# Kernel tuning notes

Measured on AMD Instinct MI355X. Metric: run time of the kernel, lower is better.

Reference implementation:

```python
import jax, jax.numpy as jnp
import numpy as np
import math

B, N, R = 1024, 50, 1000
N_POIS = 50000
D = 128
K_T = 64
K_D = 64
T_MAX = 10080.0
D_MAX = 200.0
EARTH_RADIUS_KM = 6371.0
DEG2RAD = math.pi / 180.0


def _interp_scalar(table, x):
    # Linear interpolation into 1-D table [K]; x are bin positions in [0, K-1].
    K = table.shape[0]
    x = jnp.clip(x, 0.0, K - 1 - 1e-06)
    k = jnp.floor(x).astype(jnp.int32)
    frac = x - k.astype(x.dtype)
    return (1.0 - frac) * table[k] + frac * table[jnp.minimum(k + 1, K - 1)]


def _haversine_km(lat1, lon1, lat2, lon2):
    dlat = (lat2 - lat1) * DEG2RAD
    dlon = (lon2 - lon1) * DEG2RAD
    a = jnp.sin(dlat / 2) ** 2 + jnp.cos(lat1 * DEG2RAD) * jnp.cos(lat2 * DEG2RAD) * jnp.sin(dlon / 2) ** 2
    a = jnp.clip(a, 0.0, 1.0)
    return EARTH_RADIUS_KM * 2.0 * jnp.arcsin(jnp.sqrt(a))


def setup_inputs() -> dict:
    key = jax.random.key(0)
    ks = jax.random.split(key, 16)
    poi_idx = jax.random.randint(ks[0], (B, N), 0, N_POIS)
    hour_of_week = jax.random.randint(ks[1], (B, N), 0, 169)
    lat = jax.random.uniform(ks[2], (B, N), jnp.float32)  # ~1 degree spread => up to ~150 km pairwise
    lon = jax.random.uniform(ks[3], (B, N), jnp.float32)
    t_min = jax.random.uniform(ks[4], (B, N), jnp.float32) * T_MAX
    region_centroids = jax.random.uniform(ks[5], (R, 2), jnp.float32)
    poi_emb = 0.02 * jax.random.normal(ks[6], (N_POIS + 1, D), jnp.float32)
    poi_emb = poi_emb.at[N_POIS].set(0.0)  # padding row
    time_emb = 0.02 * jax.random.normal(ks[7], (169, D), jnp.float32)
    time_emb = time_emb.at[0].set(0.0)  # padding row
    E_t = 0.1 * jax.random.normal(ks[8], (K_T,), jnp.float32)
    E_d = 0.1 * jax.random.normal(ks[9], (K_D,), jnp.float32)
    E_d_match = 0.1 * jax.random.normal(ks[10], (K_D,), jnp.float32)
    region_emb = 0.02 * jax.random.normal(ks[11], (R, D), jnp.float32)
    Wq = jax.random.normal(ks[12], (D, D), jnp.float32) / math.sqrt(D)
    Wk = jax.random.normal(ks[13], (D, D), jnp.float32) / math.sqrt(D)
    Wv = jax.random.normal(ks[14], (D, D), jnp.float32) / math.sqrt(D)
    return dict(poi_idx=poi_idx, hour_of_week=hour_of_week, lat=lat, lon=lon, t_min=t_min,
                region_centroids=region_centroids, poi_emb=poi_emb, time_emb=time_emb,
                E_t=E_t, E_d=E_d, E_d_match=E_d_match, region_emb=region_emb,
                Wq=Wq, Wk=Wk, Wv=Wv)


def reference(poi_idx, hour_of_week, lat, lon, t_min, region_centroids,
              poi_emb, time_emb, E_t, E_d, E_d_match, region_emb, Wq, Wk, Wv):
    pad_mask = poi_idx < 0  # [B, n]
    poi_safe = jnp.where(pad_mask, N_POIS, poi_idx)
    hour_safe = jnp.where(pad_mask, 0, hour_of_week)
    x = poi_emb[poi_safe] + time_emb[hour_safe]  # [B, n, D]

    # pairwise trajectory intervals [B, n, n]
    dt = jnp.abs(t_min[:, :, None] - t_min[:, None, :])
    dd = _haversine_km(lat[:, :, None], lon[:, :, None], lat[:, None, :], lon[:, None, :])
    valid = (~pad_mask).astype(x.dtype)
    valid_pair = valid[:, :, None] * valid[:, None, :]
    dt = dt * valid_pair
    dd = dd * valid_pair

    # _PairwiseBias: scalar table interpolation bias
    t_bin = jnp.clip(dt, 0.0, T_MAX) / T_MAX * (K_T - 1)
    d_bin = jnp.clip(dd, 0.0, D_MAX) / D_MAX * (K_D - 1)
    bias = _interp_scalar(E_t, t_bin) + _interp_scalar(E_d, d_bin)  # [B, n, n]

    # _SelfAttn (single head, no LN/residual, dropout=0)
    Q = x @ Wq.T
    K_ = x @ Wk.T
    V = x @ Wv.T
    scores = jnp.einsum('bnd,bmd->bnm', Q, K_) / math.sqrt(D) + bias
    scores = jnp.where(pad_mask[:, None, :], -jnp.inf, scores)
    attn = jnp.nan_to_num(jax.nn.softmax(scores, axis=-1), nan=0.0)
    S = attn @ V  # [B, n, D]

    # _MatchingLayer
    cand_lat = region_centroids[:, 0]
    cand_lon = region_centroids[:, 1]
    dd_m = _haversine_km(lat[:, :, None], lon[:, :, None], cand_lat[None, None, :], cand_lon[None, None, :])  # [B, n, R]
    dbin_m = jnp.clip(dd_m, 0.0, D_MAX) / D_MAX * (K_D - 1)
    bias_match = _interp_scalar(E_d_match, dbin_m)
    m_scores = jnp.einsum('bnd,rd->bnr', S, region_emb) / math.sqrt(D) + bias_match
    m_scores = jnp.where(pad_mask[:, :, None], -jnp.inf, m_scores)
    m_attn = jnp.nan_to_num(jax.nn.softmax(m_scores, axis=1), nan=0.0)  # softmax over trajectory dim
    scores_safe = jnp.where(pad_mask[:, :, None], 0.0, m_scores)
    return jnp.sum(m_attn * scores_safe, axis=1)  # [B, R]
```

## Files before the change

kernel.cpp:

```cpp
#include <hip/hip_runtime.h>
#include <hip/hip_bf16.h>
#include <math.h>

constexpr int BB    = 1024;
constexpr int NN    = 50;
constexpr int RR    = 1000;
constexpr int DD    = 128;
constexpr int NPOIS = 50000;
#define DEG2RADF  0.017453292519943295f
#define KHALF     0.008726646259971648f
#define RSQRTD    0.08838834764831845f
#define LOG2E     1.4426950408889634f
#define LN2       0.6931471805599453f
#define DBIN_C0   4013.7373f
#define DBIN_C1   668.95621f
#define TBIN_SC   0.00625f
#define PENAL     -1.0e30f

typedef __attribute__((ext_vector_type(8))) short bfrag8;
typedef __attribute__((ext_vector_type(4))) float f32x4;

__device__ __forceinline__ int swz128(int row, int k) {
    return row * 128 + ((((k) >> 3) ^ (row & 7)) << 3) + (k & 7);
}

__device__ __forceinline__ unsigned short f2bf(float x) {
    union { __hip_bfloat16 h; unsigned short u; } cv;
    cv.h = __float2bfloat16(x);
    return cv.u;
}

__device__ __forceinline__ float exp2_asm(float x) {
    float r;
    asm("v_exp_f32 %0, %1" : "=v"(r) : "v"(x));
    return r;
}

__device__ __forceinline__ float fract_asm(float x) {
    float r;
    asm("v_fract_f32 %0, %1" : "=v"(r) : "v"(x));
    return r;
}

__device__ __forceinline__ float cos_small(float x) {
    float x2 = x * x;
    return 1.0f - 0.5f * x2 + 0.041666667f * x2 * x2;
}

__global__ void prep_mg(const float* __restrict__ Wq, const float* __restrict__ Wk,
                        const float* __restrict__ Wv, const float* __restrict__ Re,
                        unsigned short* __restrict__ Mt, unsigned short* __restrict__ Gp) {
    int k = threadIdx.x;
    if (blockIdx.x < DD) {
        int c = blockIdx.x;
        float s0 = 0.f, s1 = 0.f, s2 = 0.f, s3 = 0.f;
        for (int d = 0; d < DD; d += 4) {
            s0 += Wq[(d + 0) * DD + k] * Wk[(d + 0) * DD + c];
            s1 += Wq[(d + 1) * DD + k] * Wk[(d + 1) * DD + c];
            s2 += Wq[(d + 2) * DD + k] * Wk[(d + 2) * DD + c];
            s3 += Wq[(d + 3) * DD + k] * Wk[(d + 3) * DD + c];
        }
        Mt[c * DD + k] = f2bf((s0 + s1 + s2 + s3) * (RSQRTD * LOG2E));
    } else {
        int r = blockIdx.x - DD;
        float val = 0.f;
        if (r < RR) {
            float s0 = 0.f, s1 = 0.f, s2 = 0.f, s3 = 0.f;
            for (int d = 0; d < DD; d += 4) {
                s0 += Wv[(d + 0) * DD + k] * Re[r * DD + d + 0];
                s1 += Wv[(d + 1) * DD + k] * Re[r * DD + d + 1];
                s2 += Wv[(d + 2) * DD + k] * Re[r * DD + d + 2];
                s3 += Wv[(d + 3) * DD + k] * Re[r * DD + d + 3];
            }
            val = (s0 + s1 + s2 + s3) * (RSQRTD * LOG2E);
        }
        int rt = r >> 6, widr = (r >> 4) & 3, colr = r & 15;
        int ks = k >> 5, quad = (k >> 3) & 3, k7 = k & 7;
        int lane = quad * 16 + colr;
        Gp[((((rt * 16 + widr * 4 + ks) * 64) + lane) << 3) + k7] = f2bf(val);
    }
}

__global__ __launch_bounds__(256) void stan_attn(
    const int* __restrict__ poi_idx, const int* __restrict__ hourw,
    const float* __restrict__ lat, const float* __restrict__ lon,
    const float* __restrict__ tmin,
    const float* __restrict__ poi_emb, const float* __restrict__ time_emb,
    const float* __restrict__ Et_g, const float* __restrict__ Ed_g,
    const unsigned short* __restrict__ Mtb, unsigned short* __restrict__ Zw) {
    __shared__ short xs[64 * 128];
    __shared__ union {
        short ys[64 * 128];
        short ps[64 * 64];
    } u2;
    __shared__ float2 Et2[64], Ed2[64];
    __shared__ float4 bnfo[64];
    __shared__ float  jpen[64];

    const int b = blockIdx.x, tid = threadIdx.x;
    const int wid = tid >> 6, lane = tid & 63;
    const int quad = lane >> 4, colr = lane & 15;

    if (tid < 64) {
        int kk = tid > 62 ? 62 : tid;
        float t0 = Et_g[kk] * LOG2E, t1 = Et_g[kk + 1] * LOG2E;
        float d0 = Ed_g[kk] * LOG2E, d1 = Ed_g[kk + 1] * LOG2E;
        Et2[tid] = make_float2(t0, t1 - t0);
        Ed2[tid] = make_float2(d0, d1 - d0);
        if (tid < NN) {
            int p = poi_idx[b * NN + tid];
            float la = lat[b * NN + tid], lo = lon[b * NN + tid];
            bnfo[tid] = make_float4(la * KHALF, lo * KHALF,
                                    cos_small(la * DEG2RADF),
                                    tmin[b * NN + tid] * TBIN_SC);
            jpen[tid] = (p < 0) ? PENAL : 0.f;
        } else {
            bnfo[tid] = make_float4(0.f, 0.f, 1.f, 0.f);
            jpen[tid] = PENAL;
        }
    }
    __syncthreads();

    for (int idx = tid; idx < 64 * 64; idx += 256) {
        int n = idx >> 6, c2 = idx & 63;
        float2 v = make_float2(0.f, 0.f);
        if (n < NN) {
            int p = poi_idx[b * NN + n];
            int pd = (p < 0);
            int ps_ = pd ? NPOIS : p;
            int hs  = pd ? 0 : hourw[b * NN + n];
            float2 pe = ((const float2*)(poi_emb  + (size_t)ps_ * DD))[c2];
            float2 te = ((const float2*)(time_emb + (size_t)hs  * DD))[c2];
            v = make_float2(pe.x + te.x, pe.y + te.y);
        }
        unsigned pack = (unsigned)f2bf(v.x) | ((unsigned)f2bf(v.y) << 16);
        ((unsigned*)xs)[n * 64 + (((c2 >> 2) ^ (n & 7)) << 2) + (c2 & 3)] = pack;
    }
    __syncthreads();

    const int q8    = (quad ^ (colr & 3)) * 8;
    const int kx    = (colr & 4) * 8;
    const int xbase = colr * 128 + q8;
    const int xe = xbase + kx, xo = xbase - kx;

    {
        f32x4 accY[2][4];
        #pragma unroll
        for (int ct = 0; ct < 2; ct++)
            #pragma unroll
            for (int mt = 0; mt < 4; mt++) accY[ct][mt] = (f32x4){0.f, 0.f, 0.f, 0.f};
        #pragma unroll
        for (int ks = 0; ks < 4; ks++) {
            const int k0 = ks * 32 + quad * 8;
            const int xoff = ((ks & 1) ? xo : xe) + ks * 32;
            bfrag8 av[4], bv[2];
            #pragma unroll
            for (int mt = 0; mt < 4; mt++)
                av[mt] = *(const bfrag8*)(&xs[xoff + mt * 2048]);
            #pragma unroll
            for (int ct = 0; ct < 2; ct++) {
                int c = wid * 32 + ct * 16 + colr;
                bv[ct] = *(const bfrag8*)(Mtb + (size_t)c * DD + k0);
            }
            #pragma unroll
            for (int ct = 0; ct < 2; ct++)
                #pragma unroll
                for (int mt = 0; mt < 4; mt++)
                    accY[ct][mt] = __builtin_amdgcn_mfma_f32_16x16x32_bf16(
                        av[mt], bv[ct], accY[ct][mt], 0, 0, 0);
        }
        #pragma unroll
        for (int ct = 0; ct < 2; ct++)
            #pragma unroll
            for (int mt = 0; mt < 4; mt++)
                #pragma unroll
                for (int reg = 0; reg < 4; reg++) {
                    int m = mt * 16 + quad * 4 + reg;
                    int c = wid * 32 + ct * 16 + colr;
                    u2.ys[swz128(m, c)] = (short)f2bf(accY[ct][mt][reg]);
                }
    }
    __syncthreads();

    const int i = wid * 16 + colr;
    const int ybase = xbase + wid * 2048;
    const int ye = ybase + kx, yo = ybase - kx;
    f32x4 accS[4];
    #pragma unroll
    for (int mt = 0; mt < 4; mt++) accS[mt] = (f32x4){0.f, 0.f, 0.f, 0.f};
    #pragma unroll
    for (int ks = 0; ks < 4; ks++) {
        const int yoff = ((ks & 1) ? yo : ye) + ks * 32;
        const int xoff = ((ks & 1) ? xo : xe) + ks * 32;
        bfrag8 bv = *(const bfrag8*)(&u2.ys[yoff]);
        #pragma unroll
        for (int mt = 0; mt < 4; mt++) {
            bfrag8 av = *(const bfrag8*)(&xs[xoff + mt * 2048]);
            accS[mt] = __builtin_amdgcn_mfma_f32_16x16x32_bf16(
                av, bv, accS[mt], 0, 0, 0);
        }
    }
    __syncthreads();

    {
        const float4 bi = bnfo[i];
        float sv[14];
        #pragma unroll
        for (int mt = 0; mt < 4; mt++) {
            const int nregs = (mt == 3) ? 2 : 4;
            #pragma unroll
            for (int reg = 0; reg < nregs; reg++) {
                int j = mt * 16 + quad * 4 + reg;
                float4 bj = bnfo[j];
                float tb = fabsf(bi.w - bj.w);
                int   kt = (int)tb;
                float ft = fract_asm(tb);
                float2 et = Et2[kt];
                float bt = fmaf(ft, et.y, et.x);
                float du = bi.x - bj.x, dv = bi.y - bj.y;
                float a = fmaf((bi.z * bj.z) * dv, dv, du * du);
                float x = __builtin_amdgcn_sqrtf(a);
                float db = x * fmaf(a, DBIN_C1, DBIN_C0);
                int   kd = (int)db;
                float fd = fract_asm(db);
                float2 ed = Ed2[kd];
                float bd = fmaf(fd, ed.y, ed.x);
                sv[mt * 4 + reg] = (accS[mt][reg] + bt) + (bd + jpen[j]);
            }
        }
        float mx = sv[0];
        #pragma unroll
        for (int t = 1; t < 14; t++) mx = fmaxf(mx, sv[t]);
        mx = fmaxf(mx, __shfl_xor(mx, 16, 64));
        mx = fmaxf(mx, __shfl_xor(mx, 32, 64));
        float l = 0.f;
        #pragma unroll
        for (int t = 0; t < 14; t++) {
            float p = exp2_asm(sv[t] - mx);
            sv[t] = p;
            l += p;
        }
        l += __shfl_xor(l, 16, 64);
        l += __shfl_xor(l, 32, 64);
        float rl = __builtin_amdgcn_rcpf(l);
        #pragma unroll
        for (int mt = 0; mt < 4; mt++)
            #pragma unroll
            for (int rp = 0; rp < 2; rp++) {
                int j0 = mt * 16 + quad * 4 + rp * 2;
                unsigned pack;
                if (mt == 3 && rp == 1) {
                    pack = 0u;
                } else {
                    unsigned lo = f2bf(sv[mt * 4 + rp * 2]     * rl);
                    unsigned hi = f2bf(sv[mt * 4 + rp * 2 + 1] * rl);
                    pack = lo | (hi << 16);
                }
                ((unsigned*)u2.ps)[i * 32 + (((j0 >> 3) ^ (i & 7)) << 2) + ((j0 & 7) >> 1)]
                    = pack;
            }
    }
    __syncthreads();

    {
        f32x4 accZ[2][4];
        #pragma unroll
        for (int nt = 0; nt < 2; nt++)
            #pragma unroll
            for (int mt = 0; mt < 4; mt++) accZ[nt][mt] = (f32x4){0.f, 0.f, 0.f, 0.f};
        union BF { unsigned u[4]; bfrag8 v; };
        const int pbase = colr * 64 + q8;
        const int pe = pbase + kx, po = pbase - kx;
        #pragma unroll
        for (int ks = 0; ks < 2; ks++) {
            const int k0 = ks * 32 + quad * 8;
            const int poff = ((ks & 1) ? po : pe) + ks * 32;
            bfrag8 av[4];
            #pragma unroll
            for (int mt = 0; mt < 4; mt++)
                av[mt] = *(const bfrag8*)(&u2.ps[poff + mt * 1024]);
            BF bvx[2];
            #pragma unroll
            for (int nt = 0; nt < 2; nt++) {
                int d = wid * 32 + nt * 16 + colr;
                #pragma unroll
                for (int t2 = 0; t2 < 4; t2++) {
                    unsigned lo = (unsigned short)xs[swz128(k0 + 2 * t2,     d)];
                    unsigned hi = (unsigned short)xs[swz128(k0 + 2 * t2 + 1, d)];
                    bvx[nt].u[t2] = lo | (hi << 16);
                }
            }
            #pragma unroll
            for (int nt = 0; nt < 2; nt++)
                #pragma unroll
                for (int mt = 0; mt < 4; mt++)
                    accZ[nt][mt] = __builtin_amdgcn_mfma_f32_16x16x32_bf16(
                        av[mt], bvx[nt].v, accZ[nt][mt], 0, 0, 0);
        }
        unsigned short* Zb = Zw + (size_t)b * NN * DD;
        #pragma unroll
        for (int mt = 0; mt < 4; mt++)
            #pragma unroll
            for (int reg = 0; reg < 4; reg++) {
                int ii = mt * 16 + quad * 4 + reg;
                if (ii < NN) {
                    #pragma unroll
                    for (int nt = 0; nt < 2; nt++) {
                        int d = wid * 32 + nt * 16 + colr;
                        Zb[(size_t)ii * DD + d] = f2bf(accZ[nt][mt][reg]);
                    }
                }
            }
    }
}

__global__ __launch_bounds__(256, 8) void stan_match(
    const unsigned short* __restrict__ Zw, const unsigned short* __restrict__ Gp,
    const float* __restrict__ cent, const float* __restrict__ Em_g,
    const int* __restrict__ poi_idx,
    const float* __restrict__ lat, const float* __restrict__ lon,
    float* __restrict__ out) {
    __shared__ short  As[64 * 128];
    __shared__ float2 Em2[64];
    __shared__ float4 Rnfo[64];
    __shared__ float4 bnfo[64];

    const int tid = threadIdx.x;
    const int b = blockIdx.x, rt = blockIdx.y;
    const int rbase = rt * 64;
    const int wid  = tid >> 6, lane = tid & 63;
    const int quad = lane >> 4, colr = lane & 15;

    if (tid < 64) {
        int kk = tid > 62 ? 62 : tid;
        float e0 = Em_g[kk] * LOG2E, e1 = Em_g[kk + 1] * LOG2E;
        Em2[tid] = make_float2(e0, e1 - e0);
        int rc = rbase + tid; if (rc > RR - 1) rc = RR - 1;
        float la = cent[rc * 2], lo = cent[rc * 2 + 1];
        Rnfo[tid] = make_float4(la * KHALF, lo * KHALF, cos_small(la * DEG2RADF), 0.f);
        if (tid < NN) {
            float bla = lat[b * NN + tid], blo = lon[b * NN + tid];
            float pen = (poi_idx[b * NN + tid] < 0) ? PENAL : 0.f;
            bnfo[tid] = make_float4(bla * KHALF, blo * KHALF,
                                    cos_small(bla * DEG2RADF), pen);
        } else {
            bnfo[tid] = make_float4(0.f, 0.f, 1.f, PENAL);
        }
    }
    {
        const int row = tid >> 2;
        uint4 z4 = make_uint4(0, 0, 0, 0);
        uint4 a0 = z4, a1 = z4, a2 = z4, a3 = z4;
        if (row < NN) {
            const uint4* src = (const uint4*)(Zw + (size_t)b * NN * DD + row * DD
                                              + (tid & 3) * 32);
            a0 = src[0]; a1 = src[1]; a2 = src[2]; a3 = src[3];
        }
        const int jb = (tid & 3) * 4, rx = row & 7;
        uint4* dstA = (uint4*)As;
        dstA[row * 16 + ((jb + 0) ^ rx)] = a0;
        dstA[row * 16 + ((jb + 1) ^ rx)] = a1;
        dstA[row * 16 + ((jb + 2) ^ rx)] = a2;
        dstA[row * 16 + ((jb + 3) ^ rx)] = a3;
    }

    const unsigned short* Gf = Gp + ((size_t)((rt * 16 + wid * 4) * 64 + lane) << 3);
    bfrag8 bfv[4];
    #pragma unroll
    for (int ks = 0; ks < 4; ks++)
        bfv[ks] = *(const bfrag8*)(Gf + ks * 512);

    __syncthreads();

    const int rL = wid * 16 + colr;
    const int r  = rbase + rL;

    const int q8    = (quad ^ (colr & 3)) * 8;
    const int kx    = (colr & 4) * 8;
    const int abase = colr * 128 + q8;
    const int ae = abase + kx, ao = abase - kx;

    f32x4 acc[4];
    #pragma unroll
    for (int mt = 0; mt < 4; mt++) acc[mt] = (f32x4){0.f, 0.f, 0.f, 0.f};

    #pragma unroll
    for (int ks = 0; ks < 4; ks++) {
        const int aoff = ((ks & 1) ? ao : ae) + ks * 32;
        #pragma unroll
        for (int mt = 0; mt < 4; mt++) {
            bfrag8 af = *(const bfrag8*)(&As[aoff + mt * 2048]);
            acc[mt] = __builtin_amdgcn_mfma_f32_16x16x32_bf16(af, bfv[ks], acc[mt], 0, 0, 0);
        }
    }

    const float4 rv = Rnfo[rL];
    float s[14];
    #pragma unroll
    for (int mt = 0; mt < 4; mt++) {
        const int nregs = (mt == 3) ? 2 : 4;
        #pragma unroll
        for (int reg = 0; reg < nregs; reg++) {
            int n = mt * 16 + quad * 4 + reg;
            float4 bn = bnfo[n];
            float du = bn.x - rv.x, dv = bn.y - rv.y;
            float a = fmaf((bn.z * rv.z) * dv, dv, du * du);
            float x = __builtin_amdgcn_sqrtf(a);
            float db = x * fmaf(a, DBIN_C1, DBIN_C0);
            int   kd = (int)db;
            float fd = fract_asm(db);
            float2 ed = Em2[kd];
            float bias = fmaf(fd, ed.y, ed.x);
            s[mt * 4 + reg] = (acc[mt][reg] + bias) + bn.w;
        }
    }
    float m = s[0];
    #pragma unroll
    for (int t = 1; t < 14; t++) m = fmaxf(m, s[t]);
    m = fmaxf(m, __shfl_xor(m, 16, 64));
    m = fmaxf(m, __shfl_xor(m, 32, 64));
    float l = 0.f, aw = 0.f;
    #pragma unroll
    for (int t = 0; t < 14; t++) {
        float p = exp2_asm(s[t] - m);
        l += p;
        aw = fmaf(p, s[t], aw);
    }
    l  += __shfl_xor(l, 16, 64); aw += __shfl_xor(aw, 16, 64);
    l  += __shfl_xor(l, 32, 64); aw += __shfl_xor(aw, 32, 64);
    if (quad == 0 && r < RR)
        out[(size_t)b * RR + r] = aw * __builtin_amdgcn_rcpf(l) * LN2;
}

extern "C" void kernel_launch(void* const* d_in, const int* in_sizes, int n_in,
                              void* d_out, int out_size, void* d_ws, size_t ws_size,
                              hipStream_t stream) {
    const int*   poi_idx  = (const int*)d_in[0];
    const int*   hourw    = (const int*)d_in[1];
    const float* lat      = (const float*)d_in[2];
    const float* lon      = (const float*)d_in[3];
    const float* tmin     = (const float*)d_in[4];
    const float* cent     = (const float*)d_in[5];
    const float* poi_emb  = (const float*)d_in[6];
    const float* time_emb = (const float*)d_in[7];
    const float* E_t      = (const float*)d_in[8];
    const float* E_d      = (const float*)d_in[9];
    const float* E_dm     = (const float*)d_in[10];
    const float* Remb     = (const float*)d_in[11];
    const float* Wq       = (const float*)d_in[12];
    const float* Wk       = (const float*)d_in[13];
    const float* Wv       = (const float*)d_in[14];
    float* out            = (float*)d_out;

    unsigned short* Mtb = (unsigned short*)d_ws;
    unsigned short* Gpb = Mtb + DD * DD;
    unsigned short* Zw  = Gpb + (size_t)1024 * DD;

    prep_mg<<<dim3(DD + 1024), DD, 0, stream>>>(Wq, Wk, Wv, Remb, Mtb, Gpb);
    stan_attn<<<dim3(BB), 256, 0, stream>>>(poi_idx, hourw, lat, lon, tmin,
                                            poi_emb, time_emb, E_t, E_d, Mtb, Zw);
    stan_match<<<dim3(BB, 16), 256, 0, stream>>>(Zw, Gpb, cent, E_dm, poi_idx, lat, lon, out);
}
```

Measured before the change: 184.8 us.

## Store Z in MFMA fragment order so match kernel reads A directly from global

The attention kernel now writes its per-batch Z output zero-padded to 64 rows and pre-swizzled into the exact bf16 MFMA A-fragment layout. The match kernel drops its LDS staging buffer and copy, and loads each A fragment straight from global memory with one 16-byte load per lane. This removes 16KB of LDS per block and the LDS write/read round trip, which should allow higher occupancy. In exchange, each of the 16 region-tile blocks per batch now rereads Z from global or L2, and the workspace per batch grows from 50 to 64 rows.

Measured after the change: 213.7 us. +15.7%, slower.

```diff
diff --git a/kernel.cpp b/kernel.cpp
--- a/kernel.cpp
+++ b/kernel.cpp
@@ -87,7 +87,7 @@
     const float* __restrict__ tmin,
     const float* __restrict__ poi_emb, const float* __restrict__ time_emb,
     const float* __restrict__ Et_g, const float* __restrict__ Ed_g,
-    const unsigned short* __restrict__ Mtb, unsigned short* __restrict__ Zw) {
+    const unsigned short* __restrict__ Mtb, unsigned short* __restrict__ Zp) {
     __shared__ short xs[64 * 128];
     __shared__ union {
         short ys[64 * 128];
@@ -297,30 +297,29 @@
                     accZ[nt][mt] = __builtin_amdgcn_mfma_f32_16x16x32_bf16(
                         av[mt], bvx[nt].v, accZ[nt][mt], 0, 0, 0);
         }
-        unsigned short* Zb = Zw + (size_t)b * NN * DD;
+        unsigned short* Zb = Zp + ((size_t)b << 13);
         #pragma unroll
         for (int mt = 0; mt < 4; mt++)
             #pragma unroll
             for (int reg = 0; reg < 4; reg++) {
                 int ii = mt * 16 + quad * 4 + reg;
-                if (ii < NN) {
-                    #pragma unroll
-                    for (int nt = 0; nt < 2; nt++) {
-                        int d = wid * 32 + nt * 16 + colr;
-                        Zb[(size_t)ii * DD + d] = f2bf(accZ[nt][mt][reg]);
-                    }
+                #pragma unroll
+                for (int nt = 0; nt < 2; nt++) {
+                    float zv = (ii < NN) ? accZ[nt][mt][reg] : 0.f;
+                    int qc = nt * 2 + (colr >> 3);
+                    Zb[(mt * 4 + wid) * 512 + (qc * 16 + quad * 4 + reg) * 8 + (colr & 7)]
+                        = f2bf(zv);
                 }
             }
     }
 }
 
 __global__ __launch_bounds__(256, 8) void stan_match(
-    const unsigned short* __restrict__ Zw, const unsigned short* __restrict__ Gp,
+    const unsigned short* __restrict__ Zp, const unsigned short* __restrict__ Gp,
     const float* __restrict__ cent, const float* __restrict__ Em_g,
     const int* __restrict__ poi_idx,
     const float* __restrict__ lat, const float* __restrict__ lon,
     float* __restrict__ out) {
-    __shared__ short  As[64 * 128];
     __shared__ float2 Em2[64];
     __shared__ float4 Rnfo[64];
     __shared__ float4 bnfo[64];
@@ -330,6 +329,12 @@
     const int rbase = rt * 64;
     const int wid  = tid >> 6, lane = tid & 63;
     const int quad = lane >> 4, colr = lane & 15;
+
+    const unsigned short* Gf = Gp + ((size_t)((rt * 16 + wid * 4) * 64 + lane) << 3);
+    bfrag8 bfv[4];
+    #pragma unroll
+    for (int ks = 0; ks < 4; ks++)
+        bfv[ks] = *(const bfrag8*)(Gf + ks * 512);
 
     if (tid < 64) {
         int kk = tid > 62 ? 62 : tid;
@@ -347,38 +352,12 @@
             bnfo[tid] = make_float4(0.f, 0.f, 1.f, PENAL);
         }
     }
-    {
-        const int row = tid >> 2;
-        uint4 z4 = make_uint4(0, 0, 0, 0);
-        uint4 a0 = z4, a1 = z4, a2 = z4, a3 = z4;
-        if (row < NN) {
-            const uint4* src = (const uint4*)(Zw + (size_t)b * NN * DD + row * DD
-                                              + (tid & 3) * 32);
-            a0 = src[0]; a1 = src[1]; a2 = src[2]; a3 = src[3];
-        }
-        const int jb = (tid & 3) * 4, rx = row & 7;
-        uint4* dstA = (uint4*)As;
-        dstA[row * 16 + ((jb + 0) ^ rx)] = a0;
-        dstA[row * 16 + ((jb + 1) ^ rx)] = a1;
-        dstA[row * 16 + ((jb + 2) ^ rx)] = a2;
-        dstA[row * 16 + ((jb + 3) ^ rx)] = a3;
-    }
-
-    const unsigned short* Gf = Gp + ((size_t)((rt * 16 + wid * 4) * 64 + lane) << 3);
-    bfrag8 bfv[4];
-    #pragma unroll
-    for (int ks = 0; ks < 4; ks++)
-        bfv[ks] = *(const bfrag8*)(Gf + ks * 512);
-
     __syncthreads();
 
     const int rL = wid * 16 + colr;
     const int r  = rbase + rL;
 
-    const int q8    = (quad ^ (colr & 3)) * 8;
-    const int kx    = (colr & 4) * 8;
-    const int abase = colr * 128 + q8;
-    const int ae = abase + kx, ao = abase - kx;
+    const unsigned short* Ab = Zp + ((size_t)b << 13) + lane * 8;
 
     f32x4 acc[4];
     #pragma unroll
@@ -386,10 +365,9 @@
 
     #pragma unroll
     for (int ks = 0; ks < 4; ks++) {
-        const int aoff = ((ks & 1) ? ao : ae) + ks * 32;
         #pragma unroll
         for (int mt = 0; mt < 4; mt++) {
-            bfrag8 af = *(const bfrag8*)(&As[aoff + mt * 2048]);
+            bfrag8 af = *(const bfrag8*)(Ab + (mt * 4 + ks) * 512);
             acc[mt] = __builtin_amdgcn_mfma_f32_16x16x32_bf16(af, bfv[ks], acc[mt], 0, 0, 0);
         }
     }
@@ -454,10 +432,10 @@
 
     unsigned short* Mtb = (unsigned short*)d_ws;
     unsigned short* Gpb = Mtb + DD * DD;
-    unsigned short* Zw  = Gpb + (size_t)1024 * DD;
+    unsigned short* Zpb = Gpb + (size_t)1024 * DD;
 
     prep_mg<<<dim3(DD + 1024), DD, 0, stream>>>(Wq, Wk, Wv, Remb, Mtb, Gpb);
     stan_attn<<<dim3(BB), 256, 0, stream>>>(poi_idx, hourw, lat, lon, tmin,
-                                            poi_emb, time_emb, E_t, E_d, Mtb, Zw);
-    stan_match<<<dim3(BB, 16), 256, 0, stream>>>(Zw, Gpb, cent, E_dm, poi_idx, lat, lon, out);
-}
+                                            poi_emb, time_emb, E_t, E_d, Mtb, Zpb);
+    stan_match<<<dim3(BB, 16), 256, 0, stream>>>(Zpb, Gpb, cent, E_dm, poi_idx, lat, lon, out);
+}
```

## Loop each match block over eight region tiles and keep A fragments in registers

Applied to the files above, without the earlier changes.

The matching kernel now gives each block one batch row and eight region tiles, instead of launching one block per (batch, tile) pair. The Z tile is staged to LDS once and its MFMA A-fragments stay in registers. The next tile's B-fragments are prefetched while the current tile runs, and region centroids are read directly rather than staged through shared memory. The softmax no longer subtracts the running max before exp2, which cuts reductions but relies on scores staying in a safe range. Fewer, longer blocks with more registers per thread (launch bounds 4) trade occupancy for less redundant Z loading and less launch overhead.

Result: no change. 181.5 us (-1.8%).

```diff
diff --git a/kernel.cpp b/kernel.cpp
--- a/kernel.cpp
+++ b/kernel.cpp
@@ -314,7 +314,7 @@
     }
 }
 
-__global__ __launch_bounds__(256, 8) void stan_match(
+__global__ __launch_bounds__(256, 4) void stan_match(
     const unsigned short* __restrict__ Zw, const unsigned short* __restrict__ Gp,
     const float* __restrict__ cent, const float* __restrict__ Em_g,
     const int* __restrict__ poi_idx,
@@ -322,22 +322,23 @@
     float* __restrict__ out) {
     __shared__ short  As[64 * 128];
     __shared__ float2 Em2[64];
-    __shared__ float4 Rnfo[64];
     __shared__ float4 bnfo[64];
 
     const int tid = threadIdx.x;
-    const int b = blockIdx.x, rt = blockIdx.y;
-    const int rbase = rt * 64;
+    const int rt0 = blockIdx.x * 8;
+    const int b   = blockIdx.y;
     const int wid  = tid >> 6, lane = tid & 63;
     const int quad = lane >> 4, colr = lane & 15;
+
+    bfrag8 bfv[4];
+    #pragma unroll
+    for (int ks = 0; ks < 4; ks++)
+        bfv[ks] = *(const bfrag8*)(Gp + (size_t)(((rt0 * 16 + wid * 4 + ks) * 64 + lane) << 3));
 
     if (tid < 64) {
         int kk = tid > 62 ? 62 : tid;
         float e0 = Em_g[kk] * LOG2E, e1 = Em_g[kk + 1] * LOG2E;
         Em2[tid] = make_float2(e0, e1 - e0);
-        int rc = rbase + tid; if (rc > RR - 1) rc = RR - 1;
-        float la = cent[rc * 2], lo = cent[rc * 2 + 1];
-        Rnfo[tid] = make_float4(la * KHALF, lo * KHALF, cos_small(la * DEG2RADF), 0.f);
         if (tid < NN) {
             float bla = lat[b * NN + tid], blo = lon[b * NN + tid];
             float pen = (poi_idx[b * NN + tid] < 0) ? PENAL : 0.f;
@@ -363,73 +364,82 @@
         dstA[row * 16 + ((jb + 2) ^ rx)] = a2;
         dstA[row * 16 + ((jb + 3) ^ rx)] = a3;
     }
-
-    const unsigned short* Gf = Gp + ((size_t)((rt * 16 + wid * 4) * 64 + lane) << 3);
-    bfrag8 bfv[4];
-    #pragma unroll
-    for (int ks = 0; ks < 4; ks++)
-        bfv[ks] = *(const bfrag8*)(Gf + ks * 512);
-
-    __syncthreads();
-
-    const int rL = wid * 16 + colr;
-    const int r  = rbase + rL;
+    __syncthreads();
 
     const int q8    = (quad ^ (colr & 3)) * 8;
     const int kx    = (colr & 4) * 8;
     const int abase = colr * 128 + q8;
     const int ae = abase + kx, ao = abase - kx;
-
-    f32x4 acc[4];
-    #pragma unroll
-    for (int mt = 0; mt < 4; mt++) acc[mt] = (f32x4){0.f, 0.f, 0.f, 0.f};
-
+    bfrag8 Af[4][4];
     #pragma unroll
     for (int ks = 0; ks < 4; ks++) {
         const int aoff = ((ks & 1) ? ao : ae) + ks * 32;
         #pragma unroll
+        for (int mt = 0; mt < 4; mt++)
+            Af[mt][ks] = *(const bfrag8*)(&As[aoff + mt * 2048]);
+    }
+
+    const int rL = wid * 16 + colr;
+
+    #pragma unroll 1
+    for (int it = 0; it < 8; it++) {
+        const int rt = rt0 + it;
+        f32x4 acc[4];
+        #pragma unroll
+        for (int mt = 0; mt < 4; mt++) acc[mt] = (f32x4){0.f, 0.f, 0.f, 0.f};
+        #pragma unroll
+        for (int ks = 0; ks < 4; ks++)
+            #pragma unroll
+            for (int mt = 0; mt < 4; mt++)
+                acc[mt] = __builtin_amdgcn_mfma_f32_16x16x32_bf16(
+                    Af[mt][ks], bfv[ks], acc[mt], 0, 0, 0);
+
+        const int rtn = (it < 7) ? rt + 1 : rt;
+        bfrag8 nxt[4];
+        #pragma unroll
+        for (int ks = 0; ks < 4; ks++)
+            nxt[ks] = *(const bfrag8*)(Gp + (size_t)(((rtn * 16 + wid * 4 + ks) * 64 + lane) << 3));
+
+        const int r  = rt * 64 + rL;
+        const int rc = (r < RR) ? r : (RR - 1);
+        float2 cc = ((const float2*)cent)[rc];
+        const float rvx = cc.x * KHALF, rvy = cc.y * KHALF;
+        const float rvz = cos_small(cc.x * DEG2RADF);
+
+        float s[14];
+        #pragma unroll
         for (int mt = 0; mt < 4; mt++) {
-            bfrag8 af = *(const bfrag8*)(&As[aoff + mt * 2048]);
-            acc[mt] = __builtin_amdgcn_mfma_f32_16x16x32_bf16(af, bfv[ks], acc[mt], 0, 0, 0);
-        }
-    }
-
-    const float4 rv = Rnfo[rL];
-    float s[14];
-    #pragma unroll
-    for (int mt = 0; mt < 4; mt++) {
-        const int nregs = (mt == 3) ? 2 : 4;
-        #pragma unroll
-        for (int reg = 0; reg < nregs; reg++) {
-            int n = mt * 16 + quad * 4 + reg;
-            float4 bn = bnfo[n];
-            float du = bn.x - rv.x, dv = bn.y - rv.y;
-            float a = fmaf((bn.z * rv.z) * dv, dv, du * du);
-            float x = __builtin_amdgcn_sqrtf(a);
-            float db = x * fmaf(a, DBIN_C1, DBIN_C0);
-            int   kd = (int)db;
-            float fd = fract_asm(db);
-            float2 ed = Em2[kd];
-            float bias = fmaf(fd, ed.y, ed.x);
-            s[mt * 4 + reg] = (acc[mt][reg] + bias) + bn.w;
-        }
-    }
-    float m = s[0];
-    #pragma unroll
-    for (int t = 1; t < 14; t++) m = fmaxf(m, s[t]);
-    m = fmaxf(m, __shfl_xor(m, 16, 64));
-    m = fmaxf(m, __shfl_xor(m, 32, 64));
-    float l = 0.f, aw = 0.f;
-    #pragma unroll
-    for (int t = 0; t < 14; t++) {
-        float p = exp2_asm(s[t] - m);
-        l += p;
-        aw = fmaf(p, s[t], aw);
-    }
-    l  += __shfl_xor(l, 16, 64); aw += __shfl_xor(aw, 16, 64);
-    l  += __shfl_xor(l, 32, 64); aw += __shfl_xor(aw, 32, 64);
-    if (quad == 0 && r < RR)
-        out[(size_t)b * RR + r] = aw * __builtin_amdgcn_rcpf(l) * LN2;
+            const int nregs = (mt == 3) ? 2 : 4;
+            #pragma unroll
+            for (int reg = 0; reg < nregs; reg++) {
+                int n = mt * 16 + quad * 4 + reg;
+                float4 bn = bnfo[n];
+                float du = bn.x - rvx, dv = bn.y - rvy;
+                float a = fmaf((bn.z * rvz) * dv, dv, du * du);
+                float x = __builtin_amdgcn_sqrtf(a);
+                float db = x * fmaf(a, DBIN_C1, DBIN_C0);
+                int   kd = (int)db;
+                float fd = fract_asm(db);
+                float2 ed = Em2[kd];
+                float bias = fmaf(fd, ed.y, ed.x);
+                s[mt * 4 + reg] = (acc[mt][reg] + bias) + bn.w;
+            }
+        }
+        float l = 0.f, aw = 0.f;
+        #pragma unroll
+        for (int t = 0; t < 14; t++) {
+            float p = exp2_asm(s[t]);
+            l += p;
+            aw = fmaf(p, s[t], aw);
+        }
+        l  += __shfl_xor(l, 16, 64); aw += __shfl_xor(aw, 16, 64);
+        l  += __shfl_xor(l, 32, 64); aw += __shfl_xor(aw, 32, 64);
+        if (quad == 0 && r < RR)
+            out[(size_t)b * RR + r] = aw * __builtin_amdgcn_rcpf(l) * LN2;
+
+        #pragma unroll
+        for (int ks = 0; ks < 4; ks++) bfv[ks] = nxt[ks];
+    }
 }
 
 extern "C" void kernel_launch(void* const* d_in, const int* in_sizes, int n_in,
@@ -459,5 +469,5 @@
     prep_mg<<<dim3(DD + 1024), DD, 0, stream>>>(Wq, Wk, Wv, Remb, Mtb, Gpb);
     stan_attn<<<dim3(BB), 256, 0, stream>>>(poi_idx, hourw, lat, lon, tmin,
                                             poi_emb, time_emb, E_t, E_d, Mtb, Zw);
-    stan_match<<<dim3(BB, 16), 256, 0, stream>>>(Zw, Gpb, cent, E_dm, poi_idx, lat, lon, out);
-}
+    stan_match<<<dim3(2, BB), 256, 0, stream>>>(Zw, Gpb, cent, E_dm, poi_idx, lat, lon, out);
+}
```
